# Kernel optimization log

Measured on AMD Instinct MI355X. Metric: run time of the kernel, lower is better.

The kernel has to match this reference:

```python
import jax, jax.numpy as jnp
import numpy as np

N, E, G = 50000, 1600000, 512
IN_DIM, HEADS, C1, C2, HIDDEN = 128, 3, 32, 32, 512
NEG_SLOPE = 0.2
EPS = 1e-16


def _glorot(key, shape):
    fan_in = shape[0]
    return jax.random.normal(key, shape, dtype=jnp.float32) / np.sqrt(fan_in)


def setup_inputs() -> dict:
    key = jax.random.key(0)
    ks = jax.random.split(key, 16)
    x = jax.random.normal(ks[0], (N, IN_DIM), dtype=jnp.float32)
    edge_index = jax.random.randint(ks[1], (2, E), 0, N, dtype=jnp.int64)
    batch = (jnp.arange(N, dtype=jnp.int64) * G) // N  # sorted, all graphs non-empty
    d1, d2 = HEADS * C1, HEADS * C2
    return {
        "x": x,
        "W_l1": _glorot(ks[2], (IN_DIM, d1)), "b_l1": jnp.zeros((d1,), jnp.float32),
        "W_r1": _glorot(ks[3], (IN_DIM, d1)), "b_r1": jnp.zeros((d1,), jnp.float32),
        "att1": _glorot(ks[4], (HEADS, C1)), "bias1": jnp.zeros((d1,), jnp.float32),
        "W_l2": _glorot(ks[5], (d1, d2)), "b_l2": jnp.zeros((d2,), jnp.float32),
        "W_r2": _glorot(ks[6], (d1, d2)), "b_r2": jnp.zeros((d2,), jnp.float32),
        "att2": _glorot(ks[7], (HEADS, C2)), "bias2": jnp.zeros((d2,), jnp.float32),
        "W_fc1": _glorot(ks[8], (d1 + d2, HIDDEN)), "b_fc1": jnp.zeros((HIDDEN,), jnp.float32),
        "W_fc2": _glorot(ks[9], (HIDDEN, 2)), "b_fc2": jnp.zeros((2,), jnp.float32),
        "edge_index": edge_index,
        "batch": batch,
    }


def gatv2_conv(xin, src, dst, W_l, b_l, W_r, b_r, att, bias, heads, out_c):
    n = xin.shape[0]
    x_l = (xin @ W_l + b_l).reshape(n, heads, out_c)  # source-side projection
    x_r = (xin @ W_r + b_r).reshape(n, heads, out_c)  # target-side projection
    e = jax.nn.leaky_relu(x_l[src] + x_r[dst], NEG_SLOPE)  # [E', H, C]
    logits = jnp.einsum("ehc,hc->eh", e, att)  # [E', H]
    m = jax.ops.segment_max(logits, dst, num_segments=n)
    a = jnp.exp(logits - m[dst])
    denom = jax.ops.segment_sum(a, dst, num_segments=n)
    alpha = a / (denom[dst] + EPS)  # per-destination edge softmax (PyG semantics)
    out = jax.ops.segment_sum(x_l[src] * alpha[:, :, None], dst, num_segments=n)
    return out.reshape(n, heads * out_c) + bias


def reference(x, W_l1, b_l1, W_r1, b_r1, att1, bias1,
              W_l2, b_l2, W_r2, b_r2, att2, bias2,
              W_fc1, b_fc1, W_fc2, b_fc2, edge_index, batch):
    n = x.shape[0]
    loop = jnp.arange(n, dtype=edge_index.dtype)
    src = jnp.concatenate([edge_index[0], loop])  # PyG GATv2Conv adds self-loops
    dst = jnp.concatenate([edge_index[1], loop])
    h1 = jnp.tanh(gatv2_conv(x, src, dst, W_l1, b_l1, W_r1, b_r1, att1, bias1, HEADS, C1))
    h2 = jnp.tanh(gatv2_conv(h1, src, dst, W_l2, b_l2, W_r2, b_r2, att2, bias2, HEADS, C2))
    h = jnp.concatenate([h1, h2], axis=1)  # [N, (C1+C2)*H]
    first_idx = jnp.searchsorted(batch, jnp.arange(G, dtype=batch.dtype))  # first node of each graph
    pooled = h[first_idx]  # [G, (C1+C2)*H]
    hidden = jax.nn.relu(pooled @ W_fc1 + b_fc1)
    logits = hidden @ W_fc2 + b_fc2
    return jax.nn.log_softmax(logits, axis=1)
```

## Files before the change

### kernel.cpp

```cpp
#include <hip/hip_runtime.h>
#include <hip/hip_bf16.h>
#include <hip/hip_fp16.h>
#include <math.h>

#define NN 50000
#define EE 1600000
#define GG 512
#define INDIM 128
#define HEADS 3
#define CC 32
#define DD 96
#define HID 512
#define NEG 0.2f
#define NEGM1 (NEG - 1.0f)
#define EPS_DEN 1e-16f
#define CAP 128
#define NBW 1568
#define LOG2E 1.44269504f
#define PCLAMP2 86.5617f

#define PS_BL1   0
#define PS_BR1   96
#define PS_ATT1  192
#define PS_BIAS1 288
#define PS_BL2   384
#define PS_BR2   480
#define PS_ATT2  576
#define PS_BIAS2 672
#define PS_BFC1  768
#define PS_WFC2  1280
#define PS_BFC2  2304
#define PS_TOTAL 2308

typedef _Float16 h8 __attribute__((ext_vector_type(8)));
typedef float f4 __attribute__((ext_vector_type(4)));

static __device__ __forceinline__ float bf2f(__hip_bfloat16 v) { return __bfloat162float(v); }

static __device__ __forceinline__ int getI(const void* p, long long i, bool w64) {
    return w64 ? ((const int*)p)[2 * i] : ((const int*)p)[i];
}

static __device__ __forceinline__ float rawf(const void* p, int i, bool isbf) {
    return isbf ? bf2f(((const __hip_bfloat16*)p)[i]) : ((const float*)p)[i];
}

static __device__ __forceinline__ void load4(const void* p, int base, int e0, bool w64, int* v) {
    const int4* q = (const int4*)p;
    if (w64) {
        int4 a = q[(base + e0) >> 1];
        int4 b = q[((base + e0) >> 1) + 1];
        v[0] = a.x; v[1] = a.z; v[2] = b.x; v[3] = b.z;
    } else {
        int4 a = q[(base + e0) >> 2];
        v[0] = a.x; v[1] = a.y; v[2] = a.z; v[3] = a.w;
    }
}

static __device__ __forceinline__ bool testbit(const unsigned* b, int i) {
    return (b[i >> 5] >> (i & 31)) & 1u;
}

template <int CTRL>
static __device__ __forceinline__ float dpp_add(float v) {
    int t = __builtin_amdgcn_update_dpp(0, __float_as_int(v), CTRL, 0xF, 0xF, true);
    return v + __int_as_float(t);
}
static __device__ __forceinline__ float red16(float p) {
    p = dpp_add<0x121>(p);
    p = dpp_add<0x122>(p);
    p = dpp_add<0x124>(p);
    p = dpp_add<0x128>(p);
    return p;
}

__global__ void detect_kernel(const void* __restrict__ x, const void* __restrict__ ei,
                              int* __restrict__ flags)
{
    __shared__ int wild, zcnt;
    if (threadIdx.x == 0) { wild = 0; zcnt = 0; }
    __syncthreads();
    int w = 0, z = 0;
    const __hip_bfloat16* xb = (const __hip_bfloat16*)x;
    for (int i = threadIdx.x; i < 4096; i += 256) {
        float v = bf2f(xb[i]);
        if (!(fabsf(v) <= 1e6f)) w++;
    }
    const int* e32 = (const int*)ei;
    for (int i = threadIdx.x; i < 4096; i += 256) {
        if (e32[2 * i + 1] == 0) z++;
    }
    atomicAdd(&wild, w);
    atomicAdd(&zcnt, z);
    __syncthreads();
    if (threadIdx.x == 0) {
        flags[0] = (wild < 64) ? 1 : 0;
        flags[1] = (zcnt > 4000) ? 1 : 0;
    }
}

struct SetupArgs {
    const void *wl1, *wr1, *wl2, *wr2, *wfc1;
    const void *bl1, *br1, *att1, *bias1, *bl2, *br2, *att2, *bias2, *bfc1, *wfc2, *bfc2;
    const void *batch;
};

__global__ void setup_kernel(SetupArgs a, const int* __restrict__ flags,
                             float* __restrict__ P, __half* __restrict__ B1,
                             __half* __restrict__ B2, __half* __restrict__ Bfc,
                             int* __restrict__ deg, int* __restrict__ needed,
                             int* __restrict__ first, unsigned* __restrict__ pb,
                             int* __restrict__ cnt)
{
    const int task = blockIdx.y;
    const int idx = blockIdx.x * 256 + threadIdx.x;
    const bool isbf = flags[0] != 0;

    if (task == 0) {
        if (idx == 0) *cnt = 0;
        if (idx >= PS_TOTAL) return;
        const void* src; int rel;
        if (idx < 768) {
            int k = idx / 96; rel = idx - k * 96;
            const void* s8[8] = {a.bl1, a.br1, a.att1, a.bias1, a.bl2, a.br2, a.att2, a.bias2};
            src = s8[k];
        } else if (idx < 1280) { src = a.bfc1; rel = idx - 768; }
        else if (idx < 2304)   { src = a.wfc2; rel = idx - 1280; }
        else if (idx < 2306)   { src = a.bfc2; rel = idx - 2304; }
        else return;
        P[idx] = rawf(src, rel, isbf);
    } else if (task == 1 || task == 2) {
        const int KC = (task == 1) ? 4 : 3;
        const int total = 12 * KC * 64;
        if (idx >= total) return;
        int lane = idx & 63, t = idx >> 6;
        int kc = t % KC, ntile = t / KC;
        int n = ntile * 16 + (lane & 15);
        int kbase = kc * 32 + (lane >> 4) * 8;
        const void* W = (task == 1) ? (n < 96 ? a.wl1 : a.wr1) : (n < 96 ? a.wl2 : a.wr2);
        int n2 = (n < 96) ? n : n - 96;
        __half* dst = ((task == 1) ? B1 : B2) + (size_t)idx * 8;
#pragma unroll
        for (int j = 0; j < 8; j++) dst[j] = __float2half(rawf(W, (kbase + j) * 96 + n2, isbf));
    } else if (task == 3) {
        const int total = 32 * 6 * 64;
        if (idx >= total) return;
        int lane = idx & 63, t = idx >> 6;
        int kc = t % 6, ntile = t / 6;
        int n = ntile * 16 + (lane & 15);
        int kbase = kc * 32 + (lane >> 4) * 8;
        __half* dst = Bfc + (size_t)idx * 8;
#pragma unroll
        for (int j = 0; j < 8; j++) dst[j] = __float2half(rawf(a.wfc1, (kbase + j) * HID + n, isbf));
    } else if (task == 4) {
        int i0 = idx * 4;
#pragma unroll
        for (int j = 0; j < 4; j++) if (i0 + j < NN) deg[i0 + j] = 0;
    } else if (task == 5) {
        if (idx >= NN) return;
        const bool w64 = flags[1] != 0;
        int b = getI(a.batch, idx, w64);
        bool isf = (idx == 0) || (getI(a.batch, idx - 1, w64) != b);
        needed[idx] = isf ? 1 : 0;
        if (isf) first[b] = idx;
    } else {
        if (idx >= NBW) return;
        const bool w64 = flags[1] != 0;
        unsigned word = 0;
        int prev = (idx == 0) ? -1 : getI(a.batch, idx * 32 - 1, w64);
        for (int bit = 0; bit < 32; bit++) {
            int i = idx * 32 + bit;
            if (i >= NN) break;
            int b = getI(a.batch, i, w64);
            if (i == 0 || b != prev) word |= (1u << bit);
            prev = b;
        }
        pb[idx] = word;
    }
}

__global__ void mark_needed_kernel(const void* __restrict__ ei, const int* __restrict__ flags,
                                   const unsigned* __restrict__ pb, int* __restrict__ needed)
{
    int e0 = (blockIdx.x * 256 + threadIdx.x) * 4;
    if (e0 >= EE) return;
    const bool w64 = flags[1] != 0;
    int d4[4];
    load4(ei, EE, e0, w64, d4);
#pragma unroll
    for (int j = 0; j < 4; j++)
        if (testbit(pb, d4[j])) needed[getI(ei, e0 + j, w64)] = 1;
}

__global__ void scatter_compact_kernel(const void* __restrict__ ei, const int* __restrict__ flags,
                                       const int* __restrict__ needed,
                                       int* __restrict__ deg, int* __restrict__ csr,
                                       int* __restrict__ list, int* __restrict__ cnt)
{
    if (blockIdx.y == 1) {
        int i = blockIdx.x * 256 + threadIdx.x;
        if (i >= NN) return;
        if (needed[i]) list[atomicAdd(cnt, 1)] = i;
        return;
    }
    int e0 = (blockIdx.x * 256 + threadIdx.x) * 4;
    if (e0 >= EE) return;
    const bool w64 = flags[1] != 0;
    int s4[4], d4[4];
    load4(ei, EE, e0, w64, d4);
    load4(ei, 0, e0, w64, s4);
#pragma unroll
    for (int j = 0; j < 4; j++) {
        int dst = d4[j];
        if (!needed[dst]) continue;
        int pos = atomicAdd(&deg[dst], 1);
        if (pos < CAP) csr[(size_t)dst * CAP + pos] = s4[j];
    }
}

template <int KDIM, int MODE>
__global__ __launch_bounds__(256) void proj_mfma_kernel(
    const void* __restrict__ Ain, const __half* __restrict__ Bswz,
    const int* __restrict__ list, const int* __restrict__ cnt,
    const float* __restrict__ P, const int* __restrict__ flags, int offBl, int offBr,
    __half* __restrict__ xl, float* __restrict__ xr)
{
    constexpr int KC = KDIM / 32;
    __shared__ __half Bs[12 * KC * 64 * 8];
    const int tid = threadIdx.x;
    const int limit = MODE ? *cnt : NN;
    const int blockBase = blockIdx.x * 64;
    if (blockBase >= limit) return;

    {
        const int chunks = 12 * KC * 64;
        for (int i = tid; i < chunks; i += 256)
            reinterpret_cast<f4*>(Bs)[i] = reinterpret_cast<const f4*>(Bswz)[i];
    }
    __syncthreads();

    const int wave = tid >> 6;
    const int lane = tid & 63;
    const int base = blockBase + wave * 16;
    if (base >= limit) return;

    const int q = lane >> 4;
    const int mlane = lane & 15;

    int aIdx = base + mlane;
    int aRow;
    if (MODE) aRow = (aIdx < limit) ? list[aIdx] : list[limit - 1];
    else      aRow = (aIdx < limit) ? aIdx : 0;

    h8 a[KC];
    if (MODE == 1) {
        const h8* arow = reinterpret_cast<const h8*>((const __half*)Ain + (size_t)aRow * KDIM);
#pragma unroll
        for (int kc = 0; kc < KC; kc++) a[kc] = arow[kc * 4 + q];
    } else if (flags[0]) {
        const int4* arow = reinterpret_cast<const int4*>((const ushort*)Ain + (size_t)aRow * KDIM);
#pragma unroll
        for (int kc = 0; kc < KC; kc++) {
            int4 r = arow[kc * 4 + q];
            int ws[4] = {r.x, r.y, r.z, r.w};
#pragma unroll
            for (int i = 0; i < 4; i++) {
                a[kc][2 * i]     = (_Float16)__int_as_float(ws[i] << 16);
                a[kc][2 * i + 1] = (_Float16)__int_as_float(ws[i] & 0xffff0000);
            }
        }
    } else {
        const f4* arow = reinterpret_cast<const f4*>((const float*)Ain + (size_t)aRow * KDIM);
#pragma unroll
        for (int kc = 0; kc < KC; kc++) {
            f4 r0 = arow[kc * 8 + q * 2];
            f4 r1 = arow[kc * 8 + q * 2 + 1];
#pragma unroll
            for (int i = 0; i < 4; i++) {
                a[kc][i]     = (_Float16)r0[i];
                a[kc][4 + i] = (_Float16)r1[i];
            }
        }
    }

    int sRow[4];
#pragma unroll
    for (int r = 0; r < 4; r++) {
        int si = base + q * 4 + r;
        sRow[r] = (si < limit) ? (MODE ? list[si] : si) : -1;
    }

    const h8* Bf = reinterpret_cast<const h8*>(Bs);
#pragma unroll
    for (int ntile = 0; ntile < 12; ntile++) {
        int n = ntile * 16 + mlane;
        float bv = (n < 96) ? P[offBl + n] : P[offBr + n - 96];
        f4 acc = {bv, bv, bv, bv};
#pragma unroll
        for (int kc = 0; kc < KC; kc++) {
            h8 b = Bf[(ntile * KC + kc) * 64 + lane];
            acc = __builtin_amdgcn_mfma_f32_16x16x32_f16(a[kc], b, acc, 0, 0, 0);
        }
#pragma unroll
        for (int r = 0; r < 4; r++) {
            if (sRow[r] < 0) continue;
            if (n < 96) xl[(size_t)sRow[r] * DD + n] = __float2half(acc[r]);
            else        xr[(size_t)sRow[r] * DD + (n - 96)] = acc[r];
        }
    }
}

template <int OUTMODE>
__global__ __launch_bounds__(256) void fused_edge_kernel(
    const int* __restrict__ csr, const int* __restrict__ deg,
    const int* __restrict__ list, const int* __restrict__ cnt,
    const __half* __restrict__ xl, const float* __restrict__ xr,
    const float* __restrict__ P, int offAtt, int offBias,
    __half* __restrict__ out)
{
    const int lane = threadIdx.x & 63;
    const int g = lane >> 4;
    const int t = lane & 15;
    const int w0 = (blockIdx.x * 256 + threadIdx.x) >> 6;
    const int nw = (gridDim.x * 256) >> 6;
    const int limit = (OUTMODE == 0) ? *cnt : GG;

    for (int li = w0; li < limit; li += nw) {
        const int n = list[li];
        const int* row = csr + (size_t)n * CAP;
        const int end = min(deg[n], CAP);
        const float* xrn = xr + (size_t)n * DD;

#pragma unroll 1
        for (int h = 0; h < HEADS; h++) {
            const int hc = h * CC + 2 * t;
            const __half2* xlb = reinterpret_cast<const __half2*>(xl + hc);

            float2 av = *reinterpret_cast<const float2*>(P + offAtt + hc);
            const float a0 = av.x * LOG2E, a1 = av.y * LOG2E;
            const float2 xr2 = *reinterpret_cast<const float2*>(xrn + hc);

            float d, o0, o1;
            {
                float2 xf = __half22float2(xlb[n * (DD / 2)]);
                float t0 = xf.x + xr2.x; t0 = fmaf(fminf(t0, 0.0f), NEGM1, t0);
                float t1 = xf.y + xr2.y; t1 = fmaf(fminf(t1, 0.0f), NEGM1, t1);
                float p = red16(fmaf(t1, a1, t0 * a0));
                float e = exp2f(fminf(p, PCLAMP2));
                if (g == 0) { d = e; o0 = e * xf.x; o1 = e * xf.y; }
                else        { d = 0.0f; o0 = 0.0f; o1 = 0.0f; }
            }

            int k = g;
            for (; k + 4 < end; k += 8) {
                int s0 = row[k], s1 = row[k + 4];
                float2 xa = __half22float2(xlb[s0 * (DD / 2)]);
                float2 xb = __half22float2(xlb[s1 * (DD / 2)]);
                float ta0 = xa.x + xr2.x; ta0 = fmaf(fminf(ta0, 0.0f), NEGM1, ta0);
                float ta1 = xa.y + xr2.y; ta1 = fmaf(fminf(ta1, 0.0f), NEGM1, ta1);
                float tb0 = xb.x + xr2.x; tb0 = fmaf(fminf(tb0, 0.0f), NEGM1, tb0);
                float tb1 = xb.y + xr2.y; tb1 = fmaf(fminf(tb1, 0.0f), NEGM1, tb1);
                float pa = red16(fmaf(ta1, a1, ta0 * a0));
                float pb2 = red16(fmaf(tb1, a1, tb0 * a0));
                float ea = exp2f(fminf(pa, PCLAMP2));
                float eb = exp2f(fminf(pb2, PCLAMP2));
                d += ea + eb;
                o0 = fmaf(ea, xa.x, o0); o0 = fmaf(eb, xb.x, o0);
                o1 = fmaf(ea, xa.y, o1); o1 = fmaf(eb, xb.y, o1);
            }
            for (; k < end; k += 4) {
                int s0 = row[k];
                float2 xa = __half22float2(xlb[s0 * (DD / 2)]);
                float ta0 = xa.x + xr2.x; ta0 = fmaf(fminf(ta0, 0.0f), NEGM1, ta0);
                float ta1 = xa.y + xr2.y; ta1 = fmaf(fminf(ta1, 0.0f), NEGM1, ta1);
                float e = exp2f(fminf(red16(fmaf(ta1, a1, ta0 * a0)), PCLAMP2));
                d += e;
                o0 = fmaf(e, xa.x, o0);
                o1 = fmaf(e, xa.y, o1);
            }

            d  += __shfl_xor(d, 16);  d  += __shfl_xor(d, 32);
            o0 += __shfl_xor(o0, 16); o0 += __shfl_xor(o0, 32);
            o1 += __shfl_xor(o1, 16); o1 += __shfl_xor(o1, 32);

            float2 bv = *reinterpret_cast<const float2*>(P + offBias + hc);
            float inv = 1.0f / (d + EPS_DEN);
            float r0 = tanhf(fmaf(o0, inv, bv.x));
            float r1 = tanhf(fmaf(o1, inv, bv.y));
            if (g == 0) {
                __half2 hv = __floats2half2_rn(r0, r1);
                if (OUTMODE == 0) *reinterpret_cast<__half2*>(out + (size_t)n * DD + hc) = hv;
                else              *reinterpret_cast<__half2*>(out + (size_t)li * DD + hc) = hv;
            }
        }
    }
}

__global__ __launch_bounds__(256) void mlp_mfma_kernel(
    const __half* __restrict__ h1h, const __half* __restrict__ A2,
    const int* __restrict__ first, const __half* __restrict__ Bfc,
    const float* __restrict__ P, const int* __restrict__ flags, void* __restrict__ outv)
{
    const int tid = threadIdx.x;
    const int wave = tid >> 6, lane = tid & 63;
    const int q = lane >> 4, ml = lane & 15;
    const int rowbase = blockIdx.x * 64 + wave * 16;
    const int g16 = rowbase + ml;

    h8 a[6];
    {
        const h8* l = reinterpret_cast<const h8*>(h1h + (size_t)first[g16] * DD);
#pragma unroll
        for (int kc = 0; kc < 3; kc++) a[kc] = l[kc * 4 + q];
        const h8* r = reinterpret_cast<const h8*>(A2 + (size_t)g16 * DD);
#pragma unroll
        for (int kc = 3; kc < 6; kc++) a[kc] = r[(kc - 3) * 4 + q];
    }

    const h8* Bf = reinterpret_cast<const h8*>(Bfc);
    const float* w2 = P + PS_WFC2;
    float p0[4] = {0, 0, 0, 0}, p1[4] = {0, 0, 0, 0};
    for (int nt = 0; nt < 32; nt++) {
        int n = nt * 16 + ml;
        float bv = P[PS_BFC1 + n];
        f4 acc = {bv, bv, bv, bv};
#pragma unroll
        for (int kc = 0; kc < 6; kc++)
            acc = __builtin_amdgcn_mfma_f32_16x16x32_f16(a[kc], Bf[(nt * 6 + kc) * 64 + lane], acc, 0, 0, 0);
        float w20 = w2[2 * n], w21 = w2[2 * n + 1];
#pragma unroll
        for (int r = 0; r < 4; r++) {
            float hdn = fmaxf(acc[r], 0.0f);
            p0[r] = fmaf(hdn, w20, p0[r]);
            p1[r] = fmaf(hdn, w21, p1[r]);
        }
    }
#pragma unroll
    for (int off = 1; off <= 8; off <<= 1) {
#pragma unroll
        for (int r = 0; r < 4; r++) {
            p0[r] += __shfl_xor(p0[r], off);
            p1[r] += __shfl_xor(p1[r], off);
        }
    }
    if (ml == 0) {
        float b0 = P[PS_BFC2], b1 = P[PS_BFC2 + 1];
#pragma unroll
        for (int r = 0; r < 4; r++) {
            int g = rowbase + q * 4 + r;
            float l0 = p0[r] + b0, l1 = p1[r] + b1;
            float mx = fmaxf(l0, l1);
            float lse = mx + logf(__expf(l0 - mx) + __expf(l1 - mx));
            if (flags[0]) {
                ((__hip_bfloat16*)outv)[g * 2 + 0] = __float2bfloat16(l0 - lse);
                ((__hip_bfloat16*)outv)[g * 2 + 1] = __float2bfloat16(l1 - lse);
            } else {
                ((float*)outv)[g * 2 + 0] = l0 - lse;
                ((float*)outv)[g * 2 + 1] = l1 - lse;
            }
        }
    }
}

extern "C" void kernel_launch(void* const* d_in, const int* in_sizes, int n_in,
                              void* d_out, int out_size, void* d_ws, size_t ws_size,
                              hipStream_t stream)
{
    const void* x     = d_in[0];
    const void* ei    = d_in[17];
    const void* batch = d_in[18];

    float* ws   = (float*)d_ws;
    float* P    = ws;
    float* xr   = P + PS_TOTAL;

    __half* hp   = (__half*)(xr + (size_t)NN * DD);
    __half* xlh  = hp;
    __half* xl2h = xlh + (size_t)NN * DD;
    __half* h1h  = xl2h + (size_t)NN * DD;
    __half* A2   = h1h + (size_t)NN * DD;
    __half* B1   = A2 + (size_t)GG * DD;
    __half* B2   = B1 + 24576;
    __half* Bfc  = B2 + 18432;

    int* ip       = (int*)(Bfc + 98304);
    int* deg      = ip;
    int* needed   = deg + NN;
    int* cnt      = needed + NN;
    int* csr      = cnt + 4;
    int* list     = csr + (size_t)NN * CAP;
    int* first    = list + NN;
    int* flags    = first + GG;
    unsigned* pb  = (unsigned*)(flags + 4);

    SetupArgs sa;
    sa.wl1 = d_in[1];  sa.bl1 = d_in[2];  sa.wr1 = d_in[3];  sa.br1 = d_in[4];
    sa.att1 = d_in[5]; sa.bias1 = d_in[6];
    sa.wl2 = d_in[7];  sa.bl2 = d_in[8];  sa.wr2 = d_in[9];  sa.br2 = d_in[10];
    sa.att2 = d_in[11]; sa.bias2 = d_in[12];
    sa.wfc1 = d_in[13]; sa.bfc1 = d_in[14]; sa.wfc2 = d_in[15]; sa.bfc2 = d_in[16];
    sa.batch = batch;

    const int edge4B = (EE / 4 + 255) / 256;
    const int mprojB = (NN + 63) / 64;
    const int fuse1B = 2048;
    const int fuse2B = GG / 4;

    detect_kernel<<<1, 256, 0, stream>>>(x, ei, flags);
    setup_kernel<<<dim3(196, 7), 256, 0, stream>>>(sa, flags, P, B1, B2, Bfc,
                                                   deg, needed, first, pb, cnt);
    mark_needed_kernel<<<edge4B, 256, 0, stream>>>(ei, flags, pb, needed);
    scatter_compact_kernel<<<dim3(edge4B, 2), 256, 0, stream>>>(ei, flags, needed,
                                                                deg, csr, list, cnt);

    proj_mfma_kernel<INDIM, 0><<<mprojB, 256, 0, stream>>>(x, B1, nullptr, nullptr,
                                                           P, flags, PS_BL1, PS_BR1, xlh, xr);
    fused_edge_kernel<0><<<fuse1B, 256, 0, stream>>>(csr, deg, list, cnt, xlh, xr,
                                                     P, PS_ATT1, PS_BIAS1, h1h);

    proj_mfma_kernel<DD, 1><<<mprojB, 256, 0, stream>>>(h1h, B2, list, cnt,
                                                        P, flags, PS_BL2, PS_BR2, xl2h, xr);
    fused_edge_kernel<1><<<fuse2B, 256, 0, stream>>>(csr, deg, first, nullptr, xl2h, xr,
                                                     P, PS_ATT2, PS_BIAS2, A2);

    mlp_mfma_kernel<<<GG / 64, 256, 0, stream>>>(h1h, A2, first, Bfc, P, flags, d_out);
}
```

Baseline: 276.2 us.

## Process all three heads per edge in one pass of the edge kernel

Fuses the per-head loop of the GATv2 edge kernel so each edge's source index is read once and all three heads' features are gathered and accumulated together. Attention weights are hoisted out of the node loop. This cuts CSR row re-reads and loop overhead and exposes more independent loads per iteration. In exchange it raises register pressure (nine accumulators plus six gathered half2 values per unrolled step), which may reduce occupancy.

```diff
diff --git a/kernel.cpp b/kernel.cpp
--- a/kernel.cpp
+++ b/kernel.cpp
@@ -72,6 +72,12 @@
     p = dpp_add<0x124>(p);
     p = dpp_add<0x128>(p);
     return p;
+}
+
+static __device__ __forceinline__ float edge_e(float2 x, float2 xr2, float2 aa) {
+    float t0 = x.x + xr2.x; t0 = fmaf(fminf(t0, 0.0f), NEGM1, t0);
+    float t1 = x.y + xr2.y; t1 = fmaf(fminf(t1, 0.0f), NEGM1, t1);
+    return exp2f(fminf(red16(fmaf(t1, aa.y, t0 * aa.x)), PCLAMP2));
 }
 
 __global__ void detect_kernel(const void* __restrict__ x, const void* __restrict__ ei,
@@ -325,73 +331,103 @@
     const int nw = (gridDim.x * 256) >> 6;
     const int limit = (OUTMODE == 0) ? *cnt : GG;
 
+    float2 a_[3];
+#pragma unroll
+    for (int h = 0; h < 3; h++) {
+        float2 av = *reinterpret_cast<const float2*>(P + offAtt + h * CC + 2 * t);
+        a_[h].x = av.x * LOG2E; a_[h].y = av.y * LOG2E;
+    }
+
     for (int li = w0; li < limit; li += nw) {
         const int n = list[li];
         const int* row = csr + (size_t)n * CAP;
         const int end = min(deg[n], CAP);
         const float* xrn = xr + (size_t)n * DD;
-
-#pragma unroll 1
-        for (int h = 0; h < HEADS; h++) {
-            const int hc = h * CC + 2 * t;
-            const __half2* xlb = reinterpret_cast<const __half2*>(xl + hc);
-
-            float2 av = *reinterpret_cast<const float2*>(P + offAtt + hc);
-            const float a0 = av.x * LOG2E, a1 = av.y * LOG2E;
-            const float2 xr2 = *reinterpret_cast<const float2*>(xrn + hc);
-
-            float d, o0, o1;
-            {
-                float2 xf = __half22float2(xlb[n * (DD / 2)]);
-                float t0 = xf.x + xr2.x; t0 = fmaf(fminf(t0, 0.0f), NEGM1, t0);
-                float t1 = xf.y + xr2.y; t1 = fmaf(fminf(t1, 0.0f), NEGM1, t1);
-                float p = red16(fmaf(t1, a1, t0 * a0));
-                float e = exp2f(fminf(p, PCLAMP2));
-                if (g == 0) { d = e; o0 = e * xf.x; o1 = e * xf.y; }
-                else        { d = 0.0f; o0 = 0.0f; o1 = 0.0f; }
+        float2 xr_[3];
+#pragma unroll
+        for (int h = 0; h < 3; h++) xr_[h] = *reinterpret_cast<const float2*>(xrn + h * CC + 2 * t);
+
+        float d0, d1, d2, o00, o01, o10, o11, o20, o21;
+        {
+            const __half2* sp = reinterpret_cast<const __half2*>(xl + (size_t)n * DD) + t;
+            float2 x0 = __half22float2(sp[0]);
+            float2 x1 = __half22float2(sp[16]);
+            float2 x2 = __half22float2(sp[32]);
+            float e0 = edge_e(x0, xr_[0], a_[0]);
+            float e1 = edge_e(x1, xr_[1], a_[1]);
+            float e2 = edge_e(x2, xr_[2], a_[2]);
+            if (g == 0) {
+                d0 = e0; o00 = e0 * x0.x; o01 = e0 * x0.y;
+                d1 = e1; o10 = e1 * x1.x; o11 = e1 * x1.y;
+                d2 = e2; o20 = e2 * x2.x; o21 = e2 * x2.y;
+            } else {
+                d0 = d1 = d2 = 0.0f;
+                o00 = o01 = o10 = o11 = o20 = o21 = 0.0f;
             }
-
-            int k = g;
-            for (; k + 4 < end; k += 8) {
-                int s0 = row[k], s1 = row[k + 4];
-                float2 xa = __half22float2(xlb[s0 * (DD / 2)]);
-                float2 xb = __half22float2(xlb[s1 * (DD / 2)]);
-                float ta0 = xa.x + xr2.x; ta0 = fmaf(fminf(ta0, 0.0f), NEGM1, ta0);
-                float ta1 = xa.y + xr2.y; ta1 = fmaf(fminf(ta1, 0.0f), NEGM1, ta1);
-                float tb0 = xb.x + xr2.x; tb0 = fmaf(fminf(tb0, 0.0f), NEGM1, tb0);
-                float tb1 = xb.y + xr2.y; tb1 = fmaf(fminf(tb1, 0.0f), NEGM1, tb1);
-                float pa = red16(fmaf(ta1, a1, ta0 * a0));
-                float pb2 = red16(fmaf(tb1, a1, tb0 * a0));
-                float ea = exp2f(fminf(pa, PCLAMP2));
-                float eb = exp2f(fminf(pb2, PCLAMP2));
-                d += ea + eb;
-                o0 = fmaf(ea, xa.x, o0); o0 = fmaf(eb, xb.x, o0);
-                o1 = fmaf(ea, xa.y, o1); o1 = fmaf(eb, xb.y, o1);
-            }
-            for (; k < end; k += 4) {
-                int s0 = row[k];
-                float2 xa = __half22float2(xlb[s0 * (DD / 2)]);
-                float ta0 = xa.x + xr2.x; ta0 = fmaf(fminf(ta0, 0.0f), NEGM1, ta0);
-                float ta1 = xa.y + xr2.y; ta1 = fmaf(fminf(ta1, 0.0f), NEGM1, ta1);
-                float e = exp2f(fminf(red16(fmaf(ta1, a1, ta0 * a0)), PCLAMP2));
-                d += e;
-                o0 = fmaf(e, xa.x, o0);
-                o1 = fmaf(e, xa.y, o1);
-            }
-
-            d  += __shfl_xor(d, 16);  d  += __shfl_xor(d, 32);
-            o0 += __shfl_xor(o0, 16); o0 += __shfl_xor(o0, 32);
-            o1 += __shfl_xor(o1, 16); o1 += __shfl_xor(o1, 32);
-
-            float2 bv = *reinterpret_cast<const float2*>(P + offBias + hc);
-            float inv = 1.0f / (d + EPS_DEN);
-            float r0 = tanhf(fmaf(o0, inv, bv.x));
-            float r1 = tanhf(fmaf(o1, inv, bv.y));
-            if (g == 0) {
-                __half2 hv = __floats2half2_rn(r0, r1);
-                if (OUTMODE == 0) *reinterpret_cast<__half2*>(out + (size_t)n * DD + hc) = hv;
-                else              *reinterpret_cast<__half2*>(out + (size_t)li * DD + hc) = hv;
-            }
+        }
+
+        int k = g;
+        for (; k + 4 < end; k += 8) {
+            int s0 = row[k], s1 = row[k + 4];
+            const __half2* p0 = reinterpret_cast<const __half2*>(xl + (size_t)s0 * DD) + t;
+            const __half2* p1 = reinterpret_cast<const __half2*>(xl + (size_t)s1 * DD) + t;
+            __half2 ra0 = p0[0], ra1 = p0[16], ra2 = p0[32];
+            __half2 rb0 = p1[0], rb1 = p1[16], rb2 = p1[32];
+            float2 xa0 = __half22float2(ra0), xa1 = __half22float2(ra1), xa2 = __half22float2(ra2);
+            float2 xb0 = __half22float2(rb0), xb1 = __half22float2(rb1), xb2 = __half22float2(rb2);
+            float ea0 = edge_e(xa0, xr_[0], a_[0]);
+            float ea1 = edge_e(xa1, xr_[1], a_[1]);
+            float ea2 = edge_e(xa2, xr_[2], a_[2]);
+            float eb0 = edge_e(xb0, xr_[0], a_[0]);
+            float eb1 = edge_e(xb1, xr_[1], a_[1]);
+            float eb2 = edge_e(xb2, xr_[2], a_[2]);
+            d0 += ea0 + eb0; d1 += ea1 + eb1; d2 += ea2 + eb2;
+            o00 = fmaf(ea0, xa0.x, o00); o00 = fmaf(eb0, xb0.x, o00);
+            o01 = fmaf(ea0, xa0.y, o01); o01 = fmaf(eb0, xb0.y, o01);
+            o10 = fmaf(ea1, xa1.x, o10); o10 = fmaf(eb1, xb1.x, o10);
+            o11 = fmaf(ea1, xa1.y, o11); o11 = fmaf(eb1, xb1.y, o11);
+            o20 = fmaf(ea2, xa2.x, o20); o20 = fmaf(eb2, xb2.x, o20);
+            o21 = fmaf(ea2, xa2.y, o21); o21 = fmaf(eb2, xb2.y, o21);
+        }
+        for (; k < end; k += 4) {
+            int s0 = row[k];
+            const __half2* p0 = reinterpret_cast<const __half2*>(xl + (size_t)s0 * DD) + t;
+            float2 xa0 = __half22float2(p0[0]);
+            float2 xa1 = __half22float2(p0[16]);
+            float2 xa2 = __half22float2(p0[32]);
+            float ea0 = edge_e(xa0, xr_[0], a_[0]);
+            float ea1 = edge_e(xa1, xr_[1], a_[1]);
+            float ea2 = edge_e(xa2, xr_[2], a_[2]);
+            d0 += ea0; d1 += ea1; d2 += ea2;
+            o00 = fmaf(ea0, xa0.x, o00); o01 = fmaf(ea0, xa0.y, o01);
+            o10 = fmaf(ea1, xa1.x, o10); o11 = fmaf(ea1, xa1.y, o11);
+            o20 = fmaf(ea2, xa2.x, o20); o21 = fmaf(ea2, xa2.y, o21);
+        }
+
+        d0 += __shfl_xor(d0, 16); d0 += __shfl_xor(d0, 32);
+        d1 += __shfl_xor(d1, 16); d1 += __shfl_xor(d1, 32);
+        d2 += __shfl_xor(d2, 16); d2 += __shfl_xor(d2, 32);
+        o00 += __shfl_xor(o00, 16); o00 += __shfl_xor(o00, 32);
+        o01 += __shfl_xor(o01, 16); o01 += __shfl_xor(o01, 32);
+        o10 += __shfl_xor(o10, 16); o10 += __shfl_xor(o10, 32);
+        o11 += __shfl_xor(o11, 16); o11 += __shfl_xor(o11, 32);
+        o20 += __shfl_xor(o20, 16); o20 += __shfl_xor(o20, 32);
+        o21 += __shfl_xor(o21, 16); o21 += __shfl_xor(o21, 32);
+
+        if (g == 0) {
+            float inv0 = 1.0f / (d0 + EPS_DEN);
+            float inv1 = 1.0f / (d1 + EPS_DEN);
+            float inv2 = 1.0f / (d2 + EPS_DEN);
+            float2 bv0 = *reinterpret_cast<const float2*>(P + offBias + 0 * CC + 2 * t);
+            float2 bv1 = *reinterpret_cast<const float2*>(P + offBias + 1 * CC + 2 * t);
+            float2 bv2 = *reinterpret_cast<const float2*>(P + offBias + 2 * CC + 2 * t);
+            __half2 h0 = __floats2half2_rn(tanhf(fmaf(o00, inv0, bv0.x)), tanhf(fmaf(o01, inv0, bv0.y)));
+            __half2 h1 = __floats2half2_rn(tanhf(fmaf(o10, inv1, bv1.x)), tanhf(fmaf(o11, inv1, bv1.y)));
+            __half2 h2 = __floats2half2_rn(tanhf(fmaf(o20, inv2, bv2.x)), tanhf(fmaf(o21, inv2, bv2.y)));
+            __half* ob = (OUTMODE == 0) ? (out + (size_t)n * DD) : (out + (size_t)li * DD);
+            *reinterpret_cast<__half2*>(ob + 0 * CC + 2 * t) = h0;
+            *reinterpret_cast<__half2*>(ob + 1 * CC + 2 * t) = h1;
+            *reinterpret_cast<__half2*>(ob + 2 * CC + 2 * t) = h2;
         }
     }
 }
```

After: 259.8 us. -6.0%, faster.
